# Kernel tuning notes

Measured on AMD Instinct MI355X. Metric: run time of the kernel, lower is better.

## Reference

```python
import jax, jax.numpy as jnp
import numpy as np

D_MODEL = 1024
N_HEADS = 16
HEAD_DIM = D_MODEL // N_HEADS
B, S = 2, 2048


def setup_inputs() -> dict:
    key = jax.random.key(0)
    ks = jax.random.split(key, 6)
    w_scale = 1.0 / np.sqrt(D_MODEL)
    return {
        "query": jax.random.normal(ks[0], (B, S, D_MODEL), dtype=jnp.float32),
        "Wq": jax.random.normal(ks[1], (D_MODEL, D_MODEL), dtype=jnp.float32) * w_scale,
        "Wk": jax.random.normal(ks[2], (D_MODEL, D_MODEL), dtype=jnp.float32) * w_scale,
        "Wv": jax.random.normal(ks[3], (D_MODEL, D_MODEL), dtype=jnp.float32) * w_scale,
        "Wo": jax.random.normal(ks[4], (D_MODEL, D_MODEL), dtype=jnp.float32) * w_scale,
        "bo": jnp.zeros((D_MODEL,), dtype=jnp.float32),
    }


def reference(query, Wq, Wk, Wv, Wo, bo):
    # Self-attention: key = value = query (forward() defaults).
    b, t, _ = query.shape
    # Q/K/V projections (nn.Linear applies x @ W.T; weights here are stored as
    # [out, in] like torch, so project with W.T). Split into heads: [B,H,T,Dh].
    def proj(x, W):
        return (x @ W.T).reshape(b, t, N_HEADS, HEAD_DIM).transpose(0, 2, 1, 3)

    q = proj(query, Wq)
    k = proj(query, Wk)
    v = proj(query, Wv)

    scale = 1.0 / np.sqrt(HEAD_DIM)
    scores = jnp.einsum("bhqd,bhkd->bhqk", q, k) * scale  # [B,H,T,T]
    # Causal mask (is_causal=True, not cross-attention).
    causal = jnp.tril(jnp.ones((t, t), dtype=bool))
    scores = jnp.where(causal, scores, jnp.finfo(scores.dtype).min)
    weights = jax.nn.softmax(scores, axis=-1)
    out = jnp.einsum("bhqk,bhkd->bhqd", weights, v)  # [B,H,T,Dh]
    out = out.transpose(0, 2, 1, 3).reshape(b, t, D_MODEL)
    # Output projection with bias (dropout is identity in eval mode).
    return out @ Wo.T + bo
```

## Files before the change

### kernel.cpp

```cpp
#include <hip/hip_runtime.h>
#include <hip/hip_bf16.h>
#include <math.h>

typedef __attribute__((ext_vector_type(8))) short short8;
typedef __attribute__((ext_vector_type(4))) float floatx4;
typedef __attribute__((ext_vector_type(2))) _Float16 half2v;
typedef __attribute__((ext_vector_type(4))) _Float16 half4v;

#define MFMA_BF16_32(a, b, c) __builtin_amdgcn_mfma_f32_16x16x32_bf16(a, b, c, 0, 0, 0)
#define MFMA_F16_16(a, b, c) __builtin_amdgcn_mfma_f32_16x16x16f16(a, b, c, 0, 0, 0)

#define PIPE_BAR4() asm volatile("s_waitcnt vmcnt(4)\n\ts_barrier" ::: "memory")
#define PIPE_BAR0() asm volatile("s_waitcnt vmcnt(0)\n\ts_barrier" ::: "memory")

static constexpr int NH = 16;
static constexpr int Bb = 2;
static constexpr int Ss = 2048;
static constexpr int DM = 1024;

__device__ inline unsigned short f2bf(float f) {
    unsigned int u = __float_as_uint(f);
    u += 0x7fffu + ((u >> 16) & 1u);
    return (unsigned short)(u >> 16);
}

__device__ __forceinline__ half2v pkrtz(float a, float b) {
    return __builtin_bit_cast(half2v, __builtin_amdgcn_cvt_pkrtz(a, b));
}

__device__ __forceinline__ void gload_lds16(const unsigned short* g, unsigned short* l) {
    __builtin_amdgcn_global_load_lds(
        (const __attribute__((address_space(1))) unsigned int*)g,
        (__attribute__((address_space(3))) unsigned int*)l, 16, 0, 0);
}

__global__ void convert_all(const float* __restrict__ X, const float* __restrict__ w0,
                            const float* __restrict__ w1, const float* __restrict__ w2,
                            const float* __restrict__ w3, unsigned short* __restrict__ dstX,
                            unsigned short* __restrict__ dstW) {
    const int bid = blockIdx.x;
    const float* src;
    unsigned short* dst;
    int i;
    if (bid < 4096) {
        src = X; dst = dstX; i = bid * 256 + threadIdx.x;
    } else {
        const int w = (bid - 4096) >> 10;
        src = (w == 0) ? w0 : (w == 1) ? w1 : (w == 2) ? w2 : w3;
        dst = dstW + (size_t)w * 1048576;
        i = ((bid - 4096) & 1023) * 256 + threadIdx.x;
    }
    float4 v = ((const float4*)src)[i];
    ushort4 o;
    o.x = f2bf(v.x); o.y = f2bf(v.y); o.z = f2bf(v.z); o.w = f2bf(v.w);
    ((ushort4*)dst)[i] = o;
}

__global__ __launch_bounds__(256, 6) void gemm_qkv(const unsigned short* __restrict__ A,
                                                   const unsigned short* __restrict__ W,
                                                   unsigned short* __restrict__ Qp,
                                                   unsigned short* __restrict__ Kp,
                                                   unsigned short* __restrict__ Vt) {
    __shared__ __align__(16) unsigned short S[2][6144];
    const int K = 1024;
    const int tid = threadIdx.x;
    const int wave = tid >> 6, lane = tid & 63;
    const int quad = lane >> 4, l16 = lane & 15;
    const int wr = wave >> 1, wc = wave & 1;

    const int lin = blockIdx.x;
    const int xcd = lin & 7, slot = lin >> 3;
    const int bxt = (xcd & 3) * 16 + (slot & 15);
    const int by = (xcd >> 2) * 12 + (slot >> 4);
    const int bm = bxt * 64;
    const int bn = by * 128;

    const int srow = tid >> 2;
    const int scg = (tid & 3) ^ ((srow >> 1) & 3);
    const unsigned short* gA0 = A + (size_t)(bm + srow) * K + scg * 8;
    const unsigned short* gB0 = W + (size_t)(bn + srow) * K + scg * 8;

    auto stage = [&](int k0, int buf) {
        gload_lds16(gA0 + k0, &S[buf][wave * 512]);
        gload_lds16(gB0 + k0, &S[buf][2048 + wave * 512]);
        gload_lds16(gB0 + (size_t)64 * K + k0, &S[buf][4096 + wave * 512]);
    };

    floatx4 acc[2][4];
#pragma unroll
    for (int i = 0; i < 2; i++)
#pragma unroll
        for (int j = 0; j < 4; j++) acc[i][j] = (floatx4)0.0f;

    stage(0, 0);
    int buf = 0;
    for (int k0 = 0; k0 < K; k0 += 32) {
        __syncthreads();
        if (k0 + 32 < K) stage(k0 + 32, buf ^ 1);
        short8 af[2];
#pragma unroll
        for (int im = 0; im < 2; im++) {
            const int frow = wr * 32 + im * 16 + l16;
            af[im] = *(const short8*)&S[buf][frow * 32 + ((quad ^ ((frow >> 1) & 3)) * 8)];
        }
#pragma unroll
        for (int jn = 0; jn < 4; jn++) {
            const int frow = wc * 64 + jn * 16 + l16;
            short8 bf = *(const short8*)&S[buf][2048 + frow * 32 +
                                               ((quad ^ ((frow >> 1) & 3)) * 8)];
#pragma unroll
            for (int im = 0; im < 2; im++) acc[im][jn] = MFMA_BF16_32(af[im], bf, acc[im][jn]);
        }
        buf ^= 1;
    }
    __syncthreads();

    if (by < 16) {
        unsigned short* LB = &S[0][0];
        unsigned short* dst = (by < 8) ? Qp : Kp;
        const int nb = (by & 7) * 128;
        const float scale = (by < 8) ? 0.125f : 1.0f;
#pragma unroll
        for (int im = 0; im < 2; im++)
#pragma unroll
            for (int jn = 0; jn < 4; jn++) {
                const int row = wr * 32 + im * 16 + quad * 4;
                const int col = wc * 64 + jn * 16 + l16;
#pragma unroll
                for (int r = 0; r < 4; r++)
                    LB[(row + r) * 132 + col] = f2bf(acc[im][jn][r] * scale);
            }
        __syncthreads();
#pragma unroll
        for (int i = 0; i < 4; ++i) {
            const int flat = i * 256 + tid;
            const int row = flat >> 4, ch = flat & 15;
            short8 v = *(const short8*)&LB[row * 132 + ch * 8];
            *(short8*)&dst[(size_t)(bm + row) * 1024 + nb + ch * 8] = v;
        }
    } else {
        _Float16* LF = (_Float16*)&S[0][0];
        const int dbase = (by - 16) * 128;
        const int bI = bm >> 11, sbase = bm & 2047;
#pragma unroll
        for (int im = 0; im < 2; im++)
#pragma unroll
            for (int jn = 0; jn < 4; jn++) {
                const int d = wc * 64 + jn * 16 + l16;
                const int sl = wr * 32 + im * 16 + quad * 4;
                *(half2v*)&LF[d * 66 + sl] = pkrtz(acc[im][jn][0], acc[im][jn][1]);
                *(half2v*)&LF[d * 66 + sl + 2] = pkrtz(acc[im][jn][2], acc[im][jn][3]);
            }
        __syncthreads();
#pragma unroll
        for (int i = 0; i < 4; ++i) {
            const int flat = i * 256 + tid;
            const int dr = flat >> 3, ch = flat & 7;
            short8 v = *(const short8*)&LF[dr * 66 + ch * 8];
            const int d = dbase + dr;
            const int head = d >> 6, d64 = d & 63;
            *(short8*)&Vt[(((size_t)(bI * 16 + head)) * 64 + d64) * 2048 + sbase + ch * 8] = v;
        }
    }
}

__global__ __launch_bounds__(256) void gemm_out(const unsigned short* __restrict__ A,
                                                const unsigned short* __restrict__ Bm,
                                                float* __restrict__ C,
                                                const float* __restrict__ bias) {
    __shared__ __align__(16) unsigned short As[2][8192];
    __shared__ __align__(16) unsigned short Bs[2][4096];
    const int K = 1024;
    const int tid = threadIdx.x;
    const int wave = tid >> 6, lane = tid & 63;
    const int quad = lane >> 4, l16 = lane & 15;

    const int l = blockIdx.x;
    const int xcd = l & 7, slot = l >> 3;
    const int bx = (xcd & 3) * 8 + (slot & 7);
    const int by = (xcd >> 2) * 8 + (slot >> 3);
    const int bm = bx * 128, bn = by * 64;

    const int s0 = wave * 64 + lane;
    const int srow = s0 >> 2;
    const int scg = (s0 & 3) ^ ((srow >> 1) & 3);
    const unsigned short* gA0 = A + (size_t)(bm + srow) * K + scg * 8;
    const unsigned short* gB0 = Bm + (size_t)(bn + srow) * K + scg * 8;

    auto stage = [&](int k0, int buf) {
#pragma unroll
        for (int kh = 0; kh < 2; ++kh) {
            gload_lds16(gA0 + k0 + kh * 32, &As[buf][kh * 4096 + wave * 512]);
            gload_lds16(gA0 + (size_t)64 * K + k0 + kh * 32,
                        &As[buf][kh * 4096 + 2048 + wave * 512]);
            gload_lds16(gB0 + k0 + kh * 32, &Bs[buf][kh * 2048 + wave * 512]);
        }
    };

    floatx4 acc[2][4];
#pragma unroll
    for (int i = 0; i < 2; i++)
#pragma unroll
        for (int j = 0; j < 4; j++) acc[i][j] = (floatx4)0.0f;

    stage(0, 0);
    int buf = 0;
    for (int k0 = 0; k0 < K; k0 += 64) {
        __syncthreads();
        if (k0 + 64 < K) stage(k0 + 64, buf ^ 1);
#pragma unroll
        for (int kh = 0; kh < 2; ++kh) {
            const int abase = kh * 4096, bbase = kh * 2048;
            short8 af[2];
#pragma unroll
            for (int im = 0; im < 2; im++) {
                const int frow = wave * 32 + im * 16 + l16;
                af[im] = *(const short8*)&As[buf][abase + frow * 32 +
                                                  ((quad ^ ((frow >> 1) & 3)) * 8)];
            }
#pragma unroll
            for (int jn = 0; jn < 4; jn++) {
                const int frow = jn * 16 + l16;
                short8 bf = *(const short8*)&Bs[buf][bbase + frow * 32 +
                                                     ((quad ^ ((frow >> 1) & 3)) * 8)];
#pragma unroll
                for (int im = 0; im < 2; im++) acc[im][jn] = MFMA_BF16_32(af[im], bf, acc[im][jn]);
            }
        }
        buf ^= 1;
    }

#pragma unroll
    for (int im = 0; im < 2; im++) {
#pragma unroll
        for (int jn = 0; jn < 4; jn++) {
            const int row0 = bm + wave * 32 + im * 16 + quad * 4;
            const int colg = bn + jn * 16 + l16;
            const float bv = bias[colg];
#pragma unroll
            for (int r = 0; r < 4; r++)
                C[(size_t)(row0 + r) * 1024 + colg] = acc[im][jn][r] + bv;
        }
    }
}

__global__ __launch_bounds__(256) void flash_attn(const unsigned short* __restrict__ Qp,
                                                  const unsigned short* __restrict__ Kp,
                                                  const _Float16* __restrict__ Vt,
                                                  unsigned short* __restrict__ Out) {
    __shared__ __align__(16) unsigned short Ks[3][4096];
    __shared__ __align__(16) _Float16 Vs[3][4096];
    const int lin = blockIdx.x;
    const int xcd = lin & 7, slot = lin >> 3;
    const int pair = xcd * 4 + ((slot >> 4) & 3);
    const int h = pair & 15, b = pair >> 4;
    const int qt0 = slot & 15;
    const int qt = ((slot >> 5) & 1) ? 15 - qt0 : qt0;

    const int tid = threadIdx.x, w = tid >> 6, lane = tid & 63;
    const int quad = lane >> 4, l16 = lane & 15;

    short8 qfA[2], qfB[2];
    {
        const unsigned short* qa =
            Qp + ((size_t)(b * 2048 + qt * 128 + w * 16 + l16) << 10) + h * 64 + quad * 8;
        qfA[0] = *(const short8*)qa;
        qfA[1] = *(const short8*)(qa + 32);
        const unsigned short* qb = qa + ((size_t)64 << 10);
        qfB[0] = *(const short8*)qb;
        qfB[1] = *(const short8*)(qb + 32);
    }

    const int t8 = tid >> 3;
    const int cg = (tid & 7) ^ (t8 & 7);
    const unsigned short* gK0 = Kp + ((size_t)(b * 2048 + t8) << 10) + h * 64 + cg * 8;
    const unsigned short* gK1 = gK0 + ((size_t)32 << 10);
    const _Float16* gV0 = Vt + ((size_t)((b * 16 + h) * 64 + t8) << 11) + cg * 8;
    const _Float16* gV1 = gV0 + ((size_t)32 << 11);
    unsigned short* ldsK = &Ks[0][0] + w * 512;
    _Float16* ldsV = &Vs[0][0] + w * 512;

    auto stage = [&](int kt, int buf) {
        const size_t ko = (size_t)kt << 16;
        const size_t vo = (size_t)kt << 6;
        gload_lds16(gK0 + ko, ldsK + buf * 4096);
        gload_lds16(gK1 + ko, ldsK + buf * 4096 + 2048);
        gload_lds16((const unsigned short*)(gV0 + vo), (unsigned short*)(ldsV + buf * 4096));
        gload_lds16((const unsigned short*)(gV1 + vo), (unsigned short*)(ldsV + buf * 4096 + 2048));
    };

    const int ktEnd = 2 * qt + 1;
    stage(0, 0);
    stage(1, 1);

    floatx4 accA[4], accB[4];
#pragma unroll
    for (int dt = 0; dt < 4; dt++) { accA[dt] = (floatx4)0.0f; accB[dt] = (floatx4)0.0f; }
    float lA = 0.0f, lB = 0.0f;
    const int qloc = w * 16 + l16;
    const int sw = l16 & 7;

    int buf = 0;
    for (int kt = 0; kt <= ktEnd; ++kt) {
        if (kt < ktEnd) { PIPE_BAR4(); } else { PIPE_BAR0(); }
        const int nbuf = (buf == 2) ? 0 : buf + 1;
        const int pbuf = (nbuf == 2) ? 0 : nbuf + 1;
        if (kt + 2 <= ktEnd) stage(kt + 2, pbuf);
        const bool aAct = (kt <= 2 * qt);
        const bool aDiag = (kt == 2 * qt);
        const bool bDiag = (kt == ktEnd);
        const unsigned short* KB = &Ks[buf][0];
        const _Float16* VB = &Vs[buf][0];

#pragma unroll
        for (int sc = 0; sc < 4; ++sc) {
            const int rowk = sc * 16 + l16;
            short8 kf0 = *(const short8*)&KB[rowk * 64 + ((quad ^ sw) * 8)];
            short8 kf1 = *(const short8*)&KB[rowk * 64 + (((4 + quad) ^ sw) * 8)];

            half4v pA, pB;
            if (aAct) {
                floatx4 sA = MFMA_BF16_32(kf0, qfA[0], (floatx4)(-2.0f));
                sA = MFMA_BF16_32(kf1, qfA[1], sA);
                float ps[4];
#pragma unroll
                for (int r = 0; r < 4; ++r) {
                    float e = __expf(sA[r]);
                    if (aDiag && (sc * 16 + quad * 4 + r > qloc)) e = 0.0f;
                    ps[r] = e;
                }
                lA += (ps[0] + ps[1]) + (ps[2] + ps[3]);
                pA = __builtin_shufflevector(pkrtz(ps[0], ps[1]), pkrtz(ps[2], ps[3]), 0, 1, 2, 3);
            }
            {
                floatx4 sB = MFMA_BF16_32(kf0, qfB[0], (floatx4)(-2.0f));
                sB = MFMA_BF16_32(kf1, qfB[1], sB);
                float ps[4];
#pragma unroll
                for (int r = 0; r < 4; ++r) {
                    float e = __expf(sB[r]);
                    if (bDiag && (sc * 16 + quad * 4 + r > qloc)) e = 0.0f;
                    ps[r] = e;
                }
                lB += (ps[0] + ps[1]) + (ps[2] + ps[3]);
                pB = __builtin_shufflevector(pkrtz(ps[0], ps[1]), pkrtz(ps[2], ps[3]), 0, 1, 2, 3);
            }

#pragma unroll
            for (int dt = 0; dt < 4; ++dt) {
                const int rowv = dt * 16 + l16;
                const int cgv = ((sc * 2 + (quad >> 1)) ^ sw);
                half4v vf = *(const half4v*)&VB[rowv * 64 + cgv * 8 + (quad & 1) * 4];
                if (aAct) accA[dt] = MFMA_F16_16(vf, pA, accA[dt]);
                accB[dt] = MFMA_F16_16(vf, pB, accB[dt]);
            }
        }
        buf = nbuf;
    }

    lA += __shfl_xor(lA, 16); lA += __shfl_xor(lA, 32);
    lB += __shfl_xor(lB, 16); lB += __shfl_xor(lB, 32);
    const float iA = 1.0f / lA;
    const float iB = 1.0f / lB;

    const size_t rowA = (size_t)(b * 2048 + qt * 128 + w * 16 + l16);
    const size_t rowB = rowA + 64;
#pragma unroll
    for (int dt = 0; dt < 4; ++dt) {
        const int col = h * 64 + dt * 16 + quad * 4;
        ushort4 oa, ob;
        oa.x = f2bf(accA[dt][0] * iA); oa.y = f2bf(accA[dt][1] * iA);
        oa.z = f2bf(accA[dt][2] * iA); oa.w = f2bf(accA[dt][3] * iA);
        ob.x = f2bf(accB[dt][0] * iB); ob.y = f2bf(accB[dt][1] * iB);
        ob.z = f2bf(accB[dt][2] * iB); ob.w = f2bf(accB[dt][3] * iB);
        *(ushort4*)&Out[rowA * 1024 + col] = oa;
        *(ushort4*)&Out[rowB * 1024 + col] = ob;
    }
}

extern "C" void kernel_launch(void* const* d_in, const int* in_sizes, int n_in,
                              void* d_out, int out_size, void* d_ws, size_t ws_size,
                              hipStream_t stream) {
    const float* X  = (const float*)d_in[0];
    const float* Wq = (const float*)d_in[1];
    const float* Wk = (const float*)d_in[2];
    const float* Wv = (const float*)d_in[3];
    const float* Wo = (const float*)d_in[4];
    const float* bo = (const float*)d_in[5];

    unsigned short* ws = (unsigned short*)d_ws;
    unsigned short* Xb   = ws;
    unsigned short* W4   = ws + (size_t)4194304;
    unsigned short* Wob  = W4 + (size_t)3145728;
    unsigned short* Qp   = ws + (size_t)8388608;
    unsigned short* Kp   = ws + (size_t)12582912;
    unsigned short* Vt   = ws + (size_t)16777216;
    unsigned short* At   = ws + (size_t)20971520;

    convert_all<<<8192, 256, 0, stream>>>(X, Wq, Wk, Wv, Wo, Xb, W4);

    gemm_qkv<<<1536, 256, 0, stream>>>(Xb, W4, Qp, Kp, Vt);

    flash_attn<<<512, 256, 0, stream>>>(Qp, Kp, (const _Float16*)Vt, At);

    gemm_out<<<512, 256, 0, stream>>>(At, Wob, (float*)d_out, bo);
}
```

Before: 187.1 us.

## Split flash attention query rows across eight waves and skip masked diagonal chunks

```diff
diff --git a/kernel.cpp b/kernel.cpp
--- a/kernel.cpp
+++ b/kernel.cpp
@@ -10,7 +10,7 @@
 #define MFMA_BF16_32(a, b, c) __builtin_amdgcn_mfma_f32_16x16x32_bf16(a, b, c, 0, 0, 0)
 #define MFMA_F16_16(a, b, c) __builtin_amdgcn_mfma_f32_16x16x16f16(a, b, c, 0, 0, 0)
 
-#define PIPE_BAR4() asm volatile("s_waitcnt vmcnt(4)\n\ts_barrier" ::: "memory")
+#define PIPE_BAR2() asm volatile("s_waitcnt vmcnt(2)\n\ts_barrier" ::: "memory")
 #define PIPE_BAR0() asm volatile("s_waitcnt vmcnt(0)\n\ts_barrier" ::: "memory")
 
 static constexpr int NH = 16;
@@ -244,10 +244,10 @@
     }
 }
 
-__global__ __launch_bounds__(256) void flash_attn(const unsigned short* __restrict__ Qp,
-                                                  const unsigned short* __restrict__ Kp,
-                                                  const _Float16* __restrict__ Vt,
-                                                  unsigned short* __restrict__ Out) {
+__global__ __launch_bounds__(512, 4) void flash_attn(const unsigned short* __restrict__ Qp,
+                                                     const unsigned short* __restrict__ Kp,
+                                                     const _Float16* __restrict__ Vt,
+                                                     unsigned short* __restrict__ Out) {
     __shared__ __align__(16) unsigned short Ks[3][4096];
     __shared__ __align__(16) _Float16 Vs[3][4096];
     const int lin = blockIdx.x;
@@ -260,23 +260,18 @@
     const int tid = threadIdx.x, w = tid >> 6, lane = tid & 63;
     const int quad = lane >> 4, l16 = lane & 15;
 
-    short8 qfA[2], qfB[2];
+    short8 qf[2];
     {
         const unsigned short* qa =
             Qp + ((size_t)(b * 2048 + qt * 128 + w * 16 + l16) << 10) + h * 64 + quad * 8;
-        qfA[0] = *(const short8*)qa;
-        qfA[1] = *(const short8*)(qa + 32);
-        const unsigned short* qb = qa + ((size_t)64 << 10);
-        qfB[0] = *(const short8*)qb;
-        qfB[1] = *(const short8*)(qb + 32);
+        qf[0] = *(const short8*)qa;
+        qf[1] = *(const short8*)(qa + 32);
     }
 
     const int t8 = tid >> 3;
     const int cg = (tid & 7) ^ (t8 & 7);
     const unsigned short* gK0 = Kp + ((size_t)(b * 2048 + t8) << 10) + h * 64 + cg * 8;
-    const unsigned short* gK1 = gK0 + ((size_t)32 << 10);
     const _Float16* gV0 = Vt + ((size_t)((b * 16 + h) * 64 + t8) << 11) + cg * 8;
-    const _Float16* gV1 = gV0 + ((size_t)32 << 11);
     unsigned short* ldsK = &Ks[0][0] + w * 512;
     _Float16* ldsV = &Vs[0][0] + w * 512;
 
@@ -284,97 +279,80 @@
         const size_t ko = (size_t)kt << 16;
         const size_t vo = (size_t)kt << 6;
         gload_lds16(gK0 + ko, ldsK + buf * 4096);
-        gload_lds16(gK1 + ko, ldsK + buf * 4096 + 2048);
         gload_lds16((const unsigned short*)(gV0 + vo), (unsigned short*)(ldsV + buf * 4096));
-        gload_lds16((const unsigned short*)(gV1 + vo), (unsigned short*)(ldsV + buf * 4096 + 2048));
     };
 
     const int ktEnd = 2 * qt + 1;
+    const int myEnd = 2 * qt + (w >> 2);
     stage(0, 0);
     stage(1, 1);
 
-    floatx4 accA[4], accB[4];
-#pragma unroll
-    for (int dt = 0; dt < 4; dt++) { accA[dt] = (floatx4)0.0f; accB[dt] = (floatx4)0.0f; }
-    float lA = 0.0f, lB = 0.0f;
-    const int qloc = w * 16 + l16;
+    floatx4 acc[4];
+#pragma unroll
+    for (int dt = 0; dt < 4; dt++) acc[dt] = (floatx4)0.0f;
+    float lsum = 0.0f;
+    const int qloc = (w & 3) * 16 + l16;
     const int sw = l16 & 7;
 
     int buf = 0;
     for (int kt = 0; kt <= ktEnd; ++kt) {
-        if (kt < ktEnd) { PIPE_BAR4(); } else { PIPE_BAR0(); }
+        if (kt < ktEnd) { PIPE_BAR2(); } else { PIPE_BAR0(); }
         const int nbuf = (buf == 2) ? 0 : buf + 1;
         const int pbuf = (nbuf == 2) ? 0 : nbuf + 1;
         if (kt + 2 <= ktEnd) stage(kt + 2, pbuf);
-        const bool aAct = (kt <= 2 * qt);
-        const bool aDiag = (kt == 2 * qt);
-        const bool bDiag = (kt == ktEnd);
-        const unsigned short* KB = &Ks[buf][0];
-        const _Float16* VB = &Vs[buf][0];
-
-#pragma unroll
-        for (int sc = 0; sc < 4; ++sc) {
-            const int rowk = sc * 16 + l16;
-            short8 kf0 = *(const short8*)&KB[rowk * 64 + ((quad ^ sw) * 8)];
-            short8 kf1 = *(const short8*)&KB[rowk * 64 + (((4 + quad) ^ sw) * 8)];
-
-            half4v pA, pB;
-            if (aAct) {
-                floatx4 sA = MFMA_BF16_32(kf0, qfA[0], (floatx4)(-2.0f));
-                sA = MFMA_BF16_32(kf1, qfA[1], sA);
-                float ps[4];
-#pragma unroll
-                for (int r = 0; r < 4; ++r) {
-                    float e = __expf(sA[r]);
-                    if (aDiag && (sc * 16 + quad * 4 + r > qloc)) e = 0.0f;
-                    ps[r] = e;
+        if (kt <= myEnd) {
+            const bool diag = (kt == myEnd);
+            const int scMax = diag ? (w & 3) : 3;
+            const unsigned short* KB = &Ks[buf][0];
+            const _Float16* VB = &Vs[buf][0];
+
+#pragma unroll
+            for (int sc = 0; sc < 4; ++sc) {
+                if (sc <= scMax) {
+                    const int rowk = sc * 16 + l16;
+                    short8 kf0 = *(const short8*)&KB[rowk * 64 + ((quad ^ sw) * 8)];
+                    short8 kf1 = *(const short8*)&KB[rowk * 64 + (((4 + quad) ^ sw) * 8)];
+
+                    floatx4 s = MFMA_BF16_32(kf0, qf[0], (floatx4)(-2.0f));
+                    s = MFMA_BF16_32(kf1, qf[1], s);
+                    float ps[4];
+#pragma unroll
+                    for (int r = 0; r < 4; ++r) {
+                        float e = __expf(s[r]);
+                        if (diag && (sc * 16 + quad * 4 + r > qloc)) e = 0.0f;
+                        ps[r] = e;
+                    }
+                    lsum += (ps[0] + ps[1]) + (ps[2] + ps[3]);
+                    half4v p = __builtin_shufflevector(pkrtz(ps[0], ps[1]),
+                                                       pkrtz(ps[2], ps[3]), 0, 1, 2, 3);
+
+#pragma unroll
+                    for (int dt = 0; dt < 4; ++dt) {
+                        const int rowv = dt * 16 + l16;
+                        const int cgv = ((sc * 2 + (quad >> 1)) ^ sw);
+                        half4v vf = *(const half4v*)&VB[rowv * 64 + cgv * 8 + (quad & 1) * 4];
+                        acc[dt] = MFMA_F16_16(vf, p, acc[dt]);
+                    }
                 }
-                lA += (ps[0] + ps[1]) + (ps[2] + ps[3]);
-                pA = __builtin_shufflevector(pkrtz(ps[0], ps[1]), pkrtz(ps[2], ps[3]), 0, 1, 2, 3);
-            }
-            {
-                floatx4 sB = MFMA_BF16_32(kf0, qfB[0], (floatx4)(-2.0f));
-                sB = MFMA_BF16_32(kf1, qfB[1], sB);
-                float ps[4];
-#pragma unroll
-                for (int r = 0; r < 4; ++r) {
-                    float e = __expf(sB[r]);
-                    if (bDiag && (sc * 16 + quad * 4 + r > qloc)) e = 0.0f;
-                    ps[r] = e;
-                }
-                lB += (ps[0] + ps[1]) + (ps[2] + ps[3]);
-                pB = __builtin_shufflevector(pkrtz(ps[0], ps[1]), pkrtz(ps[2], ps[3]), 0, 1, 2, 3);
-            }
-
-#pragma unroll
-            for (int dt = 0; dt < 4; ++dt) {
-                const int rowv = dt * 16 + l16;
-                const int cgv = ((sc * 2 + (quad >> 1)) ^ sw);
-                half4v vf = *(const half4v*)&VB[rowv * 64 + cgv * 8 + (quad & 1) * 4];
-                if (aAct) accA[dt] = MFMA_F16_16(vf, pA, accA[dt]);
-                accB[dt] = MFMA_F16_16(vf, pB, accB[dt]);
             }
         }
         buf = nbuf;
     }
 
-    lA += __shfl_xor(lA, 16); lA += __shfl_xor(lA, 32);
-    lB += __shfl_xor(lB, 16); lB += __shfl_xor(lB, 32);
-    const float iA = 1.0f / lA;
-    const float iB = 1.0f / lB;
-
-    const size_t rowA = (size_t)(b * 2048 + qt * 128 + w * 16 + l16);
-    const size_t rowB = rowA + 64;
+    lsum += __shfl_xor(lsum, 16);
+    lsum += __shfl_xor(lsum, 32);
+    const float inv = 1.0f / lsum;
+
+    const size_t row = (size_t)(b * 2048 + qt * 128 + w * 16 + l16);
 #pragma unroll
     for (int dt = 0; dt < 4; ++dt) {
         const int col = h * 64 + dt * 16 + quad * 4;
-        ushort4 oa, ob;
-        oa.x = f2bf(accA[dt][0] * iA); oa.y = f2bf(accA[dt][1] * iA);
-        oa.z = f2bf(accA[dt][2] * iA); oa.w = f2bf(accA[dt][3] * iA);
-        ob.x = f2bf(accB[dt][0] * iB); ob.y = f2bf(accB[dt][1] * iB);
-        ob.z = f2bf(accB[dt][2] * iB); ob.w = f2bf(accB[dt][3] * iB);
-        *(ushort4*)&Out[rowA * 1024 + col] = oa;
-        *(ushort4*)&Out[rowB * 1024 + col] = ob;
+        ushort4 o;
+        o.x = f2bf(acc[dt][0] * inv);
+        o.y = f2bf(acc[dt][1] * inv);
+        o.z = f2bf(acc[dt][2] * inv);
+        o.w = f2bf(acc[dt][3] * inv);
+        *(ushort4*)&Out[row * 1024 + col] = o;
     }
 }
 
@@ -401,7 +379,7 @@
 
     gemm_qkv<<<1536, 256, 0, stream>>>(Xb, W4, Qp, Kp, Vt);
 
-    flash_attn<<<512, 256, 0, stream>>>(Qp, Kp, (const _Float16*)Vt, At);
+    flash_attn<<<512, 512, 0, stream>>>(Qp, Kp, (const _Float16*)Vt, At);
 
     gemm_out<<<512, 256, 0, stream>>>(At, Wob, (float*)d_out, bo);
 }
```

Result: faster. 182.9 us (-2.3%).
